# Kernel tuning notes

Hardware: AMD Instinct MI355X
Metric: run time of the kernel (lower is better)

Reference implementation:

```python
import jax, jax.numpy as jnp
import numpy as np

# module hyperparams (init_kwargs)
OUTLINER_RATIO_1 = 0.01
OUTLINER_RATIO_2 = 0.01
SUB_OUTLINER_RATIO_2 = 0.2
SUB_OUTLINER_BIT_2 = 8
RANK = 16


def setup_inputs() -> dict:
    key = jax.random.key(0)
    k1, k2 = jax.random.split(key)
    B, H, S, D = 2, 16, 2048, 128
    # x1 is a softmax output (attention probabilities): rows sum to 1, values in [0,1]
    logits = jax.random.normal(k1, (B, H, S, S), dtype=jnp.float32)
    x1 = jax.nn.softmax(logits, axis=-1)
    x2 = jax.random.normal(k2, (B, H, S, D), dtype=jnp.float32)
    return {"x1": x1, "x2": x2}


def get_statistics_softmax(x, outliner_ratio):
    # kth-value threshold on first batch element (torch.kthvalue, 1-indexed)
    v = jnp.sort(x[0].reshape(-1))
    k = int(v.size * (1.0 - outliner_ratio))
    return v[k - 1]


def get_statistics_x2(x, outliner_ratio, sub_ratio, bit):
    x0 = x[0]  # [H, S, D]
    D = x0.shape[-1]
    a = jnp.abs(x0).reshape(-1)
    k = int(a.size * (1.0 - outliner_ratio))
    outliner = jnp.sort(a)[k - 1]
    # residual after removing outliers; rank columns by L2 norm
    resid = jnp.where(jnp.abs(x0) > outliner, 0.0, x0).reshape(-1, D)
    col_norm = jnp.linalg.norm(resid, axis=0)  # [D]
    n_cols = max(1, int(sub_ratio * D))
    _, cols = jax.lax.top_k(col_norm, n_cols)  # max-norm column list (static size)
    sub = resid[:, cols]
    qmax = float(2 ** (bit - 1) - 1)
    scale = jnp.max(jnp.abs(sub)) / qmax
    return outliner, cols, scale


def prune_softmax(x, outliner):
    return jnp.where(x > outliner, x, 0.0)


def fake_divide_outliner_suboutlinear_svd(x, outliner, cols, scale, rank, bit):
    # 1) split out outliers (kept exactly)
    x_out = jnp.where(jnp.abs(x) > outliner, x, 0.0)
    r = x - x_out
    # 2) rank-`rank` SVD approximation of the residual (batched over B,H)
    U, Sv, Vt = jnp.linalg.svd(r, full_matrices=False)
    x_lr = (U[..., :rank] * Sv[..., None, :rank]) @ Vt[..., :rank, :]
    r2 = r - x_lr
    # 3) fake-quantize the high-norm (sub-outlier) columns at `bit` bits; drop the rest
    qmax = float(2 ** (bit - 1) - 1)
    sub_q = jnp.clip(jnp.round(r2[..., cols] / scale), -qmax - 1.0, qmax) * scale
    r_q = jnp.zeros_like(r2).at[..., cols].set(sub_q)
    return x_out + x_lr + r_q


def reference(x1, x2):
    # iteration = 0 (< 10): compute statistics branch of EfficientMemoryGEMMWithSoftmaxFunc.forward
    result = x1 @ x2
    outliner_1 = get_statistics_softmax(x1, OUTLINER_RATIO_1)
    outliner_2, cols_2, scale_2 = get_statistics_x2(
        x2, OUTLINER_RATIO_2, SUB_OUTLINER_RATIO_2, SUB_OUTLINER_BIT_2)
    # The pruned/compressed tensors are computed (saved for backward in torch);
    # forward output matches Func.forward's returns.
    _x1p = prune_softmax(x1, outliner_1)
    _x2c = fake_divide_outliner_suboutlinear_svd(
        x2, outliner_2, cols_2, scale_2, RANK, SUB_OUTLINER_BIT_2)
    return (result, outliner_1, outliner_2, cols_2, scale_2)
```

## Files before the change

### kernel.cpp

```cpp
#include <hip/hip_runtime.h>

typedef __bf16 bf16x8 __attribute__((ext_vector_type(8)));
typedef unsigned short u16x8 __attribute__((ext_vector_type(8)));
typedef float f32x4 __attribute__((ext_vector_type(4)));

#define S_DIM 2048
#define D_DIM 128
#define N1 67108864LL
#define N2 4194304LL
#define RANK1 66437774u
#define RANK2 4152359u

#define OUT_O1 8388608
#define OUT_O2 8388609
#define OUT_COLS 8388610
#define OUT_SCALE 8388635

#define WS_H0 0
#define WS_H1 2048
#define WS_H2 4096
#define WS_H3 6144
#define WS_STATE 6656
#define WS_SMAX 6660
#define WS_MASK 6664
#define WS_SUMSQ 6672
#define WS_TOTAL 8192

__device__ __forceinline__ unsigned short f2bf(float f) {
  unsigned u = __float_as_uint(f);
  return (unsigned short)((u + 0x7FFFu + ((u >> 16) & 1u)) >> 16);
}

__device__ __forceinline__ unsigned long long pack4(float x, float y, float z, float w) {
  return (unsigned long long)f2bf(x)
       | ((unsigned long long)f2bf(y) << 16)
       | ((unsigned long long)f2bf(z) << 32)
       | ((unsigned long long)f2bf(w) << 48);
}

__global__ void init_ws(unsigned* __restrict__ ws) {
  int i = blockIdx.x * 256 + threadIdx.x;
  if (i < WS_TOTAL) ws[i] = (i == WS_STATE) ? RANK2 : 0u;
}

#define LDA 40

__global__ __launch_bounds__(256, 2) void gemm_kernel(
    const float* __restrict__ x1, const float* __restrict__ x2,
    float* __restrict__ out, unsigned* __restrict__ hist) {
  __shared__ __align__(16) unsigned short lA[128 * LDA];
  __shared__ __align__(16) unsigned short lB[128 * LDA];
  __shared__ unsigned lh[4][2048];

  const int bid = blockIdx.x;
  const int bh = (bid & 7) + ((bid >> 7) << 3);
  const int mt = (bid >> 3) & 15;
  const int t = threadIdx.x;
  const int lane = t & 63;
  const int wave = t >> 6;
  const int wm = (wave >> 1) * 64;
  const int wn = (wave & 1) * 64;
  const int l15 = lane & 15;
  const int quad = lane >> 4;
  const bool do_hist = (bh < 16);

  unsigned* myh = lh[wave];
  if (do_hist) {
    for (int i = lane; i < 2048; i += 64) myh[i] = 0u;
  }

  const float* Ag = x1 + (long long)bh * S_DIM * S_DIM + (long long)mt * 128 * S_DIM;
  const float* Bg = x2 + (long long)bh * S_DIM * D_DIM;
  float* Cg = out + (long long)bh * S_DIM * D_DIM + (long long)mt * 128 * D_DIM;

  f32x4 acc[4][4];
#pragma unroll
  for (int i = 0; i < 4; ++i)
#pragma unroll
    for (int j = 0; j < 4; ++j) acc[i][j] = f32x4{0.f, 0.f, 0.f, 0.f};

  const int a_seg = t & 7;
  const int a_row = t >> 3;
  const int b_n = t & 127;
  const int b_kq = t >> 7;

  float4 a_r[4];
  float4 b_r[4];
#pragma unroll
  for (int p = 0; p < 4; ++p)
    a_r[p] = *reinterpret_cast<const float4*>(Ag + (long long)(a_row + p * 32) * S_DIM + a_seg * 4);
#pragma unroll
  for (int g = 0; g < 4; ++g) {
    int k0 = b_kq * 16 + g * 4;
    long long base = (long long)k0 * D_DIM + b_n;
    b_r[g].x = Bg[base];
    b_r[g].y = Bg[base + D_DIM];
    b_r[g].z = Bg[base + 2 * D_DIM];
    b_r[g].w = Bg[base + 3 * D_DIM];
  }

  for (int kb = 0; kb < S_DIM; kb += 32) {
#pragma unroll
    for (int p = 0; p < 4; ++p) {
      int row = a_row + p * 32;
      *reinterpret_cast<unsigned long long*>(&lA[row * LDA + a_seg * 4]) =
          pack4(a_r[p].x, a_r[p].y, a_r[p].z, a_r[p].w);
    }
#pragma unroll
    for (int g = 0; g < 4; ++g) {
      int k0 = b_kq * 16 + g * 4;
      *reinterpret_cast<unsigned long long*>(&lB[b_n * LDA + k0]) =
          pack4(b_r[g].x, b_r[g].y, b_r[g].z, b_r[g].w);
    }

    if (do_hist) {
#pragma unroll
      for (int p = 0; p < 4; ++p) {
        atomicAdd(&myh[__float_as_uint(a_r[p].x) >> 19], 1u);
        atomicAdd(&myh[__float_as_uint(a_r[p].y) >> 19], 1u);
        atomicAdd(&myh[__float_as_uint(a_r[p].z) >> 19], 1u);
        atomicAdd(&myh[__float_as_uint(a_r[p].w) >> 19], 1u);
      }
    }

    if (kb + 32 < S_DIM) {
#pragma unroll
      for (int p = 0; p < 4; ++p)
        a_r[p] = *reinterpret_cast<const float4*>(
            Ag + (long long)(a_row + p * 32) * S_DIM + (kb + 32) + a_seg * 4);
#pragma unroll
      for (int g = 0; g < 4; ++g) {
        int k0 = b_kq * 16 + g * 4;
        long long base = (long long)(kb + 32 + k0) * D_DIM + b_n;
        b_r[g].x = Bg[base];
        b_r[g].y = Bg[base + D_DIM];
        b_r[g].z = Bg[base + 2 * D_DIM];
        b_r[g].w = Bg[base + 3 * D_DIM];
      }
    }
    __syncthreads();

    bf16x8 af[4], bfr[4];
#pragma unroll
    for (int i = 0; i < 4; ++i) {
      af[i] = __builtin_bit_cast(bf16x8,
          *reinterpret_cast<const u16x8*>(&lA[(wm + i * 16 + l15) * LDA + quad * 8]));
      bfr[i] = __builtin_bit_cast(bf16x8,
          *reinterpret_cast<const u16x8*>(&lB[(wn + i * 16 + l15) * LDA + quad * 8]));
    }
#pragma unroll
    for (int i = 0; i < 4; ++i)
#pragma unroll
      for (int j = 0; j < 4; ++j)
        acc[i][j] = __builtin_amdgcn_mfma_f32_16x16x32_bf16(af[i], bfr[j], acc[i][j], 0, 0, 0);
    __syncthreads();
  }

#pragma unroll
  for (int i = 0; i < 4; ++i) {
#pragma unroll
    for (int j = 0; j < 4; ++j) {
      int row0 = wm + i * 16 + quad * 4;
      int col = wn + j * 16 + l15;
#pragma unroll
      for (int r = 0; r < 4; ++r)
        Cg[(long long)(row0 + r) * D_DIM + col] = acc[i][j][r];
    }
  }

  if (do_hist) {
    for (int i = t; i < 2048; i += 256) {
      unsigned s = lh[0][i] + lh[1][i] + lh[2][i] + lh[3][i];
      if (s) atomicAdd(&hist[i], s);
    }
  }
}

__global__ void x1_select(const unsigned* __restrict__ hist, float* __restrict__ out) {
  __shared__ unsigned ps[256];
  const int t = threadIdx.x;
  unsigned v[8];
  unsigned s = 0;
#pragma unroll
  for (int j = 0; j < 8; ++j) { v[j] = hist[t * 8 + j]; s += v[j]; }
  ps[t] = s;
  __syncthreads();
  for (int off = 1; off < 256; off <<= 1) {
    unsigned add = (t >= off) ? ps[t - off] : 0u;
    __syncthreads();
    ps[t] += add;
    __syncthreads();
  }
  unsigned incl = ps[t];
  unsigned before = incl - s;
  if (RANK1 >= before && RANK1 < incl) {
    unsigned rr = RANK1 - before;
    for (int j = 0; j < 8; ++j) {
      if (rr < v[j]) {
        unsigned b = (unsigned)(t * 8 + j);
        float lo = __uint_as_float(b << 19);
        float hi = __uint_as_float((b + 1u) << 19);
        out[OUT_O1] = lo + (hi - lo) * (((float)rr + 0.5f) / (float)v[j]);
        break;
      }
      rr -= v[j];
    }
  }
}

__global__ void x2_hist(const float* __restrict__ x2, unsigned* __restrict__ h,
                        const unsigned* __restrict__ state, int phase) {
  __shared__ unsigned lh[2048];
  const int nb = (phase == 3) ? 512 : 2048;
  for (int i = threadIdx.x; i < nb; i += 256) lh[i] = 0u;
  __syncthreads();
  const unsigned b1 = state[1];
  const unsigned pfx2 = (state[1] << 11) | state[2];
  long long i0 = (long long)(blockIdx.x * 256 + threadIdx.x) * 4;
  long long stride = (long long)gridDim.x * 1024;
  for (long long i = i0; i < N2; i += stride) {
    float4 v = *reinterpret_cast<const float4*>(x2 + i);
    float fv[4] = {v.x, v.y, v.z, v.w};
#pragma unroll
    for (int j = 0; j < 4; ++j) {
      unsigned key = __float_as_uint(fv[j]) & 0x7FFFFFFFu;
      if (phase == 1) {
        atomicAdd(&lh[key >> 20], 1u);
      } else if (phase == 2) {
        if ((key >> 20) == b1) atomicAdd(&lh[(key >> 9) & 0x7FFu], 1u);
      } else {
        if ((key >> 9) == pfx2) atomicAdd(&lh[key & 0x1FFu], 1u);
      }
    }
  }
  __syncthreads();
  for (int i = threadIdx.x; i < nb; i += 256)
    if (lh[i]) atomicAdd(&h[i], lh[i]);
}

__global__ void x2_scan(const unsigned* __restrict__ h, unsigned* state,
                        float* __restrict__ out, int phase) {
  __shared__ unsigned ps[256];
  const int nb = (phase == 3) ? 512 : 2048;
  const int per = nb >> 8;
  const int t = threadIdx.x;
  const unsigned r = state[0];
  const unsigned sb1 = state[1];
  const unsigned sb2 = state[2];
  unsigned v[8];
  unsigned s = 0;
  for (int j = 0; j < per; ++j) { v[j] = h[t * per + j]; s += v[j]; }
  ps[t] = s;
  __syncthreads();
  for (int off = 1; off < 256; off <<= 1) {
    unsigned add = (t >= off) ? ps[t - off] : 0u;
    __syncthreads();
    ps[t] += add;
    __syncthreads();
  }
  unsigned incl = ps[t];
  unsigned before = incl - s;
  if (r >= before && r < incl) {
    unsigned rr = r - before;
    for (int j = 0; j < per; ++j) {
      if (rr < v[j]) {
        unsigned b = (unsigned)(t * per + j);
        state[0] = rr;
        if (phase == 1) state[1] = b;
        else if (phase == 2) state[2] = b;
        else {
          unsigned bits = (sb1 << 20) | (sb2 << 9) | b;
          state[3] = bits;
          out[OUT_O2] = __uint_as_float(bits);
        }
        break;
      }
      rr -= v[j];
    }
  }
}

__global__ void colnorm_kernel(const float* __restrict__ x2,
                               const unsigned* __restrict__ state,
                               float* __restrict__ sumsq) {
  const float thr = __uint_as_float(state[3]);
  const int t = threadIdx.x;
  const int c = t & 127;
  const int half = t >> 7;
  float local = 0.f;
  for (int i = 0; i < 64; ++i) {
    int row = blockIdx.x * 128 + i * 2 + half;
    float x = x2[(long long)row * 128 + c];
    if (fabsf(x) <= thr) local += x * x;
  }
  __shared__ float red[256];
  red[t] = local;
  __syncthreads();
  if (half == 0) atomicAdd(&sumsq[c], red[c] + red[c + 128]);
}

__global__ void topk_kernel(const float* __restrict__ sumsq, float* __restrict__ out,
                            unsigned* __restrict__ mask) {
  __shared__ float v[128];
  __shared__ float rv[128];
  __shared__ int ri[128];
  __shared__ unsigned msk[4];
  const int t = threadIdx.x;
  v[t] = sumsq[t];
  if (t < 4) msk[t] = 0u;
  __syncthreads();
  for (int s = 0; s < 25; ++s) {
    rv[t] = v[t];
    ri[t] = t;
    __syncthreads();
    for (int off = 64; off >= 1; off >>= 1) {
      if (t < off) {
        float a = rv[t], b = rv[t + off];
        int ia = ri[t], ib = ri[t + off];
        if (b > a || (b == a && ib < ia)) { rv[t] = b; ri[t] = ib; }
      }
      __syncthreads();
    }
    if (t == 0) {
      int c = ri[0];
      out[OUT_COLS + s] = (float)c;
      v[c] = -1.0f;
      msk[c >> 5] |= 1u << (c & 31);
    }
    __syncthreads();
  }
  if (t < 4) mask[t] = msk[t];
}

__global__ void scale_kernel(const float* __restrict__ x2,
                             const unsigned* __restrict__ state,
                             const unsigned* __restrict__ mask,
                             unsigned* __restrict__ smax) {
  const float thr = __uint_as_float(state[3]);
  unsigned long long mlo = (unsigned long long)mask[0] | ((unsigned long long)mask[1] << 32);
  unsigned long long mhi = (unsigned long long)mask[2] | ((unsigned long long)mask[3] << 32);
  long long i0 = (long long)(blockIdx.x * 256 + threadIdx.x) * 4;
  long long stride = (long long)gridDim.x * 1024;
  float best = 0.f;
  for (long long i = i0; i < N2; i += stride) {
    float4 v = *reinterpret_cast<const float4*>(x2 + i);
    float fv[4] = {v.x, v.y, v.z, v.w};
    int cbase = (int)(i & 127);
#pragma unroll
    for (int j = 0; j < 4; ++j) {
      int c = cbase + j;
      unsigned long long w = (c < 64) ? mlo : mhi;
      if ((w >> (c & 63)) & 1ULL) {
        float a = fabsf(fv[j]);
        if (a <= thr && a > best) best = a;
      }
    }
  }
  __shared__ float red[256];
  red[threadIdx.x] = best;
  __syncthreads();
  for (int off = 128; off >= 1; off >>= 1) {
    if (threadIdx.x < off) red[threadIdx.x] = fmaxf(red[threadIdx.x], red[threadIdx.x + off]);
    __syncthreads();
  }
  if (threadIdx.x == 0) atomicMax(smax, __float_as_uint(red[0]));
}

__global__ void finalize_kernel(const unsigned* __restrict__ smax, float* __restrict__ out) {
  out[OUT_SCALE] = __uint_as_float(*smax) / 127.0f;
}

extern "C" void kernel_launch(void* const* d_in, const int* in_sizes, int n_in,
                              void* d_out, int out_size, void* d_ws, size_t ws_size,
                              hipStream_t stream) {
  (void)in_sizes; (void)n_in; (void)out_size; (void)ws_size;
  const float* x1 = (const float*)d_in[0];
  const float* x2 = (const float*)d_in[1];
  float* out = (float*)d_out;
  unsigned* ws = (unsigned*)d_ws;

  init_ws<<<32, 256, 0, stream>>>(ws);
  gemm_kernel<<<512, 256, 0, stream>>>(x1, x2, out, ws + WS_H0);
  x1_select<<<1, 256, 0, stream>>>(ws + WS_H0, out);
  x2_hist<<<256, 256, 0, stream>>>(x2, ws + WS_H1, ws + WS_STATE, 1);
  x2_scan<<<1, 256, 0, stream>>>(ws + WS_H1, ws + WS_STATE, out, 1);
  x2_hist<<<256, 256, 0, stream>>>(x2, ws + WS_H2, ws + WS_STATE, 2);
  x2_scan<<<1, 256, 0, stream>>>(ws + WS_H2, ws + WS_STATE, out, 2);
  x2_hist<<<256, 256, 0, stream>>>(x2, ws + WS_H3, ws + WS_STATE, 3);
  x2_scan<<<1, 256, 0, stream>>>(ws + WS_H3, ws + WS_STATE, out, 3);
  colnorm_kernel<<<256, 256, 0, stream>>>(x2, ws + WS_STATE, (float*)(ws + WS_SUMSQ));
  topk_kernel<<<1, 128, 0, stream>>>((const float*)(ws + WS_SUMSQ), out, ws + WS_MASK);
  scale_kernel<<<256, 256, 0, stream>>>(x2, ws + WS_STATE, ws + WS_MASK, ws + WS_SMAX);
  finalize_kernel<<<1, 1, 0, stream>>>(ws + WS_SMAX, out);
}
```

Before: 843.4 us.

## Fuse statistics kernels via last-block tickets and fold x2 histogram into GEMM

```diff
diff --git a/kernel.cpp b/kernel.cpp
--- a/kernel.cpp
+++ b/kernel.cpp
@@ -21,21 +21,15 @@
 #define WS_H2 4096
 #define WS_H3 6144
 #define WS_STATE 6656
-#define WS_SMAX 6660
-#define WS_MASK 6664
 #define WS_SUMSQ 6672
+#define WS_CMAX 6800
+#define WS_TICKET 6928
 #define WS_TOTAL 8192
 
-__device__ __forceinline__ unsigned short f2bf(float f) {
-  unsigned u = __float_as_uint(f);
-  return (unsigned short)((u + 0x7FFFu + ((u >> 16) & 1u)) >> 16);
-}
-
-__device__ __forceinline__ unsigned long long pack4(float x, float y, float z, float w) {
-  return (unsigned long long)f2bf(x)
-       | ((unsigned long long)f2bf(y) << 16)
-       | ((unsigned long long)f2bf(z) << 32)
-       | ((unsigned long long)f2bf(w) << 48);
+__device__ __forceinline__ unsigned long long pack4c(float x, float y, float z, float w) {
+  union { unsigned long long u; __bf16 h[4]; } cv;
+  cv.h[0] = (__bf16)x; cv.h[1] = (__bf16)y; cv.h[2] = (__bf16)z; cv.h[3] = (__bf16)w;
+  return cv.u;
 }
 
 __global__ void init_ws(unsigned* __restrict__ ws) {
@@ -47,10 +41,13 @@
 
 __global__ __launch_bounds__(256, 2) void gemm_kernel(
     const float* __restrict__ x1, const float* __restrict__ x2,
-    float* __restrict__ out, unsigned* __restrict__ hist) {
+    float* __restrict__ out, unsigned* __restrict__ ws) {
   __shared__ __align__(16) unsigned short lA[128 * LDA];
   __shared__ __align__(16) unsigned short lB[128 * LDA];
   __shared__ unsigned lh[4][2048];
+  __shared__ unsigned lh2[2048];
+  __shared__ unsigned ps[256];
+  __shared__ unsigned lastt;
 
   const int bid = blockIdx.x;
   const int bh = (bid & 7) + ((bid >> 7) << 3);
@@ -67,7 +64,9 @@
   unsigned* myh = lh[wave];
   if (do_hist) {
     for (int i = lane; i < 2048; i += 64) myh[i] = 0u;
-  }
+    for (int i = t; i < 2048; i += 256) lh2[i] = 0u;
+  }
+  __syncthreads();
 
   const float* Ag = x1 + (long long)bh * S_DIM * S_DIM + (long long)mt * 128 * S_DIM;
   const float* Bg = x2 + (long long)bh * S_DIM * D_DIM;
@@ -81,61 +80,71 @@
 
   const int a_seg = t & 7;
   const int a_row = t >> 3;
-  const int b_n = t & 127;
+  const int bcol = t & 127;
   const int b_kq = t >> 7;
 
-  float4 a_r[4];
-  float4 b_r[4];
+  float4 a_c[4], b_c[4];
 #pragma unroll
   for (int p = 0; p < 4; ++p)
-    a_r[p] = *reinterpret_cast<const float4*>(Ag + (long long)(a_row + p * 32) * S_DIM + a_seg * 4);
+    a_c[p] = *reinterpret_cast<const float4*>(Ag + (long long)(a_row + p * 32) * S_DIM + a_seg * 4);
 #pragma unroll
   for (int g = 0; g < 4; ++g) {
     int k0 = b_kq * 16 + g * 4;
-    long long base = (long long)k0 * D_DIM + b_n;
-    b_r[g].x = Bg[base];
-    b_r[g].y = Bg[base + D_DIM];
-    b_r[g].z = Bg[base + 2 * D_DIM];
-    b_r[g].w = Bg[base + 3 * D_DIM];
+    long long base = (long long)k0 * D_DIM + bcol;
+    b_c[g].x = Bg[base];
+    b_c[g].y = Bg[base + D_DIM];
+    b_c[g].z = Bg[base + 2 * D_DIM];
+    b_c[g].w = Bg[base + 3 * D_DIM];
   }
 
   for (int kb = 0; kb < S_DIM; kb += 32) {
+    float4 a_p[4], b_p[4];
+    const bool pf = (kb + 32 < S_DIM);
+    if (pf) {
+#pragma unroll
+      for (int p = 0; p < 4; ++p)
+        a_p[p] = *reinterpret_cast<const float4*>(
+            Ag + (long long)(a_row + p * 32) * S_DIM + (kb + 32) + a_seg * 4);
+#pragma unroll
+      for (int g = 0; g < 4; ++g) {
+        int k0 = b_kq * 16 + g * 4;
+        long long base = (long long)(kb + 32 + k0) * D_DIM + bcol;
+        b_p[g].x = Bg[base];
+        b_p[g].y = Bg[base + D_DIM];
+        b_p[g].z = Bg[base + 2 * D_DIM];
+        b_p[g].w = Bg[base + 3 * D_DIM];
+      }
+    }
+
 #pragma unroll
     for (int p = 0; p < 4; ++p) {
       int row = a_row + p * 32;
       *reinterpret_cast<unsigned long long*>(&lA[row * LDA + a_seg * 4]) =
-          pack4(a_r[p].x, a_r[p].y, a_r[p].z, a_r[p].w);
+          pack4c(a_c[p].x, a_c[p].y, a_c[p].z, a_c[p].w);
     }
 #pragma unroll
     for (int g = 0; g < 4; ++g) {
       int k0 = b_kq * 16 + g * 4;
-      *reinterpret_cast<unsigned long long*>(&lB[b_n * LDA + k0]) =
-          pack4(b_r[g].x, b_r[g].y, b_r[g].z, b_r[g].w);
+      *reinterpret_cast<unsigned long long*>(&lB[bcol * LDA + k0]) =
+          pack4c(b_c[g].x, b_c[g].y, b_c[g].z, b_c[g].w);
     }
 
     if (do_hist) {
 #pragma unroll
       for (int p = 0; p < 4; ++p) {
-        atomicAdd(&myh[__float_as_uint(a_r[p].x) >> 19], 1u);
-        atomicAdd(&myh[__float_as_uint(a_r[p].y) >> 19], 1u);
-        atomicAdd(&myh[__float_as_uint(a_r[p].z) >> 19], 1u);
-        atomicAdd(&myh[__float_as_uint(a_r[p].w) >> 19], 1u);
-      }
-    }
-
-    if (kb + 32 < S_DIM) {
-#pragma unroll
-      for (int p = 0; p < 4; ++p)
-        a_r[p] = *reinterpret_cast<const float4*>(
-            Ag + (long long)(a_row + p * 32) * S_DIM + (kb + 32) + a_seg * 4);
-#pragma unroll
-      for (int g = 0; g < 4; ++g) {
-        int k0 = b_kq * 16 + g * 4;
-        long long base = (long long)(kb + 32 + k0) * D_DIM + b_n;
-        b_r[g].x = Bg[base];
-        b_r[g].y = Bg[base + D_DIM];
-        b_r[g].z = Bg[base + 2 * D_DIM];
-        b_r[g].w = Bg[base + 3 * D_DIM];
+        atomicAdd(&myh[__float_as_uint(a_c[p].x) >> 19], 1u);
+        atomicAdd(&myh[__float_as_uint(a_c[p].y) >> 19], 1u);
+        atomicAdd(&myh[__float_as_uint(a_c[p].z) >> 19], 1u);
+        atomicAdd(&myh[__float_as_uint(a_c[p].w) >> 19], 1u);
+      }
+      if ((kb >> 7) == mt) {
+#pragma unroll
+        for (int g = 0; g < 4; ++g) {
+          atomicAdd(&lh2[(__float_as_uint(b_c[g].x) & 0x7FFFFFFFu) >> 20], 1u);
+          atomicAdd(&lh2[(__float_as_uint(b_c[g].y) & 0x7FFFFFFFu) >> 20], 1u);
+          atomicAdd(&lh2[(__float_as_uint(b_c[g].z) & 0x7FFFFFFFu) >> 20], 1u);
+          atomicAdd(&lh2[(__float_as_uint(b_c[g].w) & 0x7FFFFFFFu) >> 20], 1u);
+        }
       }
     }
     __syncthreads();
@@ -154,6 +163,13 @@
       for (int j = 0; j < 4; ++j)
         acc[i][j] = __builtin_amdgcn_mfma_f32_16x16x32_bf16(af[i], bfr[j], acc[i][j], 0, 0, 0);
     __syncthreads();
+
+    if (pf) {
+#pragma unroll
+      for (int p = 0; p < 4; ++p) a_c[p] = a_p[p];
+#pragma unroll
+      for (int g = 0; g < 4; ++g) b_c[g] = b_p[g];
+    }
   }
 
 #pragma unroll
@@ -171,52 +187,91 @@
   if (do_hist) {
     for (int i = t; i < 2048; i += 256) {
       unsigned s = lh[0][i] + lh[1][i] + lh[2][i] + lh[3][i];
-      if (s) atomicAdd(&hist[i], s);
-    }
-  }
-}
-
-__global__ void x1_select(const unsigned* __restrict__ hist, float* __restrict__ out) {
+      if (s) atomicAdd(&ws[WS_H0 + i], s);
+      unsigned s2 = lh2[i];
+      if (s2) atomicAdd(&ws[WS_H1 + i], s2);
+    }
+  }
+  __threadfence();
+  __syncthreads();
+  if (t == 0) lastt = atomicAdd(&ws[WS_TICKET + 0], 1u);
+  __syncthreads();
+  if (lastt != 511u) return;
+
+  {
+    unsigned v[8];
+    unsigned s = 0;
+#pragma unroll
+    for (int j = 0; j < 8; ++j) { v[j] = atomicAdd(&ws[WS_H0 + t * 8 + j], 0u); s += v[j]; }
+    ps[t] = s;
+    __syncthreads();
+    for (int off = 1; off < 256; off <<= 1) {
+      unsigned add = (t >= off) ? ps[t - off] : 0u;
+      __syncthreads();
+      ps[t] += add;
+      __syncthreads();
+    }
+    unsigned incl = ps[t];
+    unsigned before = incl - s;
+    if (RANK1 >= before && RANK1 < incl) {
+      unsigned rr = RANK1 - before;
+      for (int j = 0; j < 8; ++j) {
+        if (rr < v[j]) {
+          unsigned b = (unsigned)(t * 8 + j);
+          float lo = __uint_as_float(b << 19);
+          float hi = __uint_as_float((b + 1u) << 19);
+          out[OUT_O1] = lo + (hi - lo) * (((float)rr + 0.5f) / (float)v[j]);
+          break;
+        }
+        rr -= v[j];
+      }
+    }
+  }
+  __syncthreads();
+
+  {
+    unsigned v[8];
+    unsigned s = 0;
+#pragma unroll
+    for (int j = 0; j < 8; ++j) { v[j] = atomicAdd(&ws[WS_H1 + t * 8 + j], 0u); s += v[j]; }
+    ps[t] = s;
+    __syncthreads();
+    for (int off = 1; off < 256; off <<= 1) {
+      unsigned add = (t >= off) ? ps[t - off] : 0u;
+      __syncthreads();
+      ps[t] += add;
+      __syncthreads();
+    }
+    unsigned incl = ps[t];
+    unsigned before = incl - s;
+    if (RANK2 >= before && RANK2 < incl) {
+      unsigned rr = RANK2 - before;
+      for (int j = 0; j < 8; ++j) {
+        if (rr < v[j]) {
+          ws[WS_STATE + 0] = rr;
+          ws[WS_STATE + 1] = (unsigned)(t * 8 + j);
+          break;
+        }
+        rr -= v[j];
+      }
+    }
+  }
+}
+
+__global__ void x2_pass(const float* __restrict__ x2, unsigned* __restrict__ ws,
+                        float* __restrict__ out, int phase) {
+  __shared__ unsigned lh[2048];
   __shared__ unsigned ps[256];
+  __shared__ unsigned lastt;
+  unsigned* h = ws + ((phase == 2) ? WS_H2 : WS_H3);
+  unsigned* state = ws + WS_STATE;
+  const int nb = (phase == 3) ? 512 : 2048;
   const int t = threadIdx.x;
-  unsigned v[8];
-  unsigned s = 0;
-#pragma unroll
-  for (int j = 0; j < 8; ++j) { v[j] = hist[t * 8 + j]; s += v[j]; }
-  ps[t] = s;
-  __syncthreads();
-  for (int off = 1; off < 256; off <<= 1) {
-    unsigned add = (t >= off) ? ps[t - off] : 0u;
-    __syncthreads();
-    ps[t] += add;
-    __syncthreads();
-  }
-  unsigned incl = ps[t];
-  unsigned before = incl - s;
-  if (RANK1 >= before && RANK1 < incl) {
-    unsigned rr = RANK1 - before;
-    for (int j = 0; j < 8; ++j) {
-      if (rr < v[j]) {
-        unsigned b = (unsigned)(t * 8 + j);
-        float lo = __uint_as_float(b << 19);
-        float hi = __uint_as_float((b + 1u) << 19);
-        out[OUT_O1] = lo + (hi - lo) * (((float)rr + 0.5f) / (float)v[j]);
-        break;
-      }
-      rr -= v[j];
-    }
-  }
-}
-
-__global__ void x2_hist(const float* __restrict__ x2, unsigned* __restrict__ h,
-                        const unsigned* __restrict__ state, int phase) {
-  __shared__ unsigned lh[2048];
-  const int nb = (phase == 3) ? 512 : 2048;
-  for (int i = threadIdx.x; i < nb; i += 256) lh[i] = 0u;
+  for (int i = t; i < nb; i += 256) lh[i] = 0u;
   __syncthreads();
   const unsigned b1 = state[1];
   const unsigned pfx2 = (state[1] << 11) | state[2];
-  long long i0 = (long long)(blockIdx.x * 256 + threadIdx.x) * 4;
+  long long i0 = (long long)(blockIdx.x * 256 + t) * 4;
   long long stride = (long long)gridDim.x * 1024;
   for (long long i = i0; i < N2; i += stride) {
     float4 v = *reinterpret_cast<const float4*>(x2 + i);
@@ -224,9 +279,7 @@
 #pragma unroll
     for (int j = 0; j < 4; ++j) {
       unsigned key = __float_as_uint(fv[j]) & 0x7FFFFFFFu;
-      if (phase == 1) {
-        atomicAdd(&lh[key >> 20], 1u);
-      } else if (phase == 2) {
+      if (phase == 2) {
         if ((key >> 20) == b1) atomicAdd(&lh[(key >> 9) & 0x7FFu], 1u);
       } else {
         if ((key >> 9) == pfx2) atomicAdd(&lh[key & 0x1FFu], 1u);
@@ -234,22 +287,21 @@
     }
   }
   __syncthreads();
-  for (int i = threadIdx.x; i < nb; i += 256)
+  for (int i = t; i < nb; i += 256)
     if (lh[i]) atomicAdd(&h[i], lh[i]);
-}
-
-__global__ void x2_scan(const unsigned* __restrict__ h, unsigned* state,
-                        float* __restrict__ out, int phase) {
-  __shared__ unsigned ps[256];
-  const int nb = (phase == 3) ? 512 : 2048;
+  __threadfence();
+  __syncthreads();
+  if (t == 0) lastt = atomicAdd(&ws[WS_TICKET + ((phase == 2) ? 1 : 2)], 1u);
+  __syncthreads();
+  if (lastt != 255u) return;
+
   const int per = nb >> 8;
-  const int t = threadIdx.x;
   const unsigned r = state[0];
   const unsigned sb1 = state[1];
   const unsigned sb2 = state[2];
   unsigned v[8];
   unsigned s = 0;
-  for (int j = 0; j < per; ++j) { v[j] = h[t * per + j]; s += v[j]; }
+  for (int j = 0; j < per; ++j) { v[j] = atomicAdd(&h[t * per + j], 0u); s += v[j]; }
   ps[t] = s;
   __syncthreads();
   for (int off = 1; off < 256; off <<= 1) {
@@ -265,10 +317,10 @@
     for (int j = 0; j < per; ++j) {
       if (rr < v[j]) {
         unsigned b = (unsigned)(t * per + j);
-        state[0] = rr;
-        if (phase == 1) state[1] = b;
-        else if (phase == 2) state[2] = b;
-        else {
+        if (phase == 2) {
+          state[0] = rr;
+          state[2] = b;
+        } else {
           unsigned bits = (sb1 << 20) | (sb2 << 9) | b;
           state[3] = bits;
           out[OUT_O2] = __uint_as_float(bits);
@@ -280,38 +332,56 @@
   }
 }
 
-__global__ void colnorm_kernel(const float* __restrict__ x2,
-                               const unsigned* __restrict__ state,
-                               float* __restrict__ sumsq) {
+__global__ void colnorm_kernel(const float* __restrict__ x2, unsigned* __restrict__ ws,
+                               float* __restrict__ out) {
+  __shared__ float red[256];
+  __shared__ unsigned redm[256];
+  __shared__ float vv[128];
+  __shared__ float rv[128];
+  __shared__ int ri[128];
+  __shared__ unsigned cmv[128];
+  __shared__ unsigned lastt;
+  unsigned* state = ws + WS_STATE;
+  float* sumsq = (float*)(ws + WS_SUMSQ);
+  unsigned* cmax = ws + WS_CMAX;
   const float thr = __uint_as_float(state[3]);
   const int t = threadIdx.x;
   const int c = t & 127;
   const int half = t >> 7;
   float local = 0.f;
+  unsigned lmax = 0u;
   for (int i = 0; i < 64; ++i) {
     int row = blockIdx.x * 128 + i * 2 + half;
     float x = x2[(long long)row * 128 + c];
-    if (fabsf(x) <= thr) local += x * x;
-  }
-  __shared__ float red[256];
+    float a = fabsf(x);
+    if (a <= thr) {
+      local += x * x;
+      unsigned ab = __float_as_uint(a);
+      if (ab > lmax) lmax = ab;
+    }
+  }
   red[t] = local;
-  __syncthreads();
-  if (half == 0) atomicAdd(&sumsq[c], red[c] + red[c + 128]);
-}
-
-__global__ void topk_kernel(const float* __restrict__ sumsq, float* __restrict__ out,
-                            unsigned* __restrict__ mask) {
-  __shared__ float v[128];
-  __shared__ float rv[128];
-  __shared__ int ri[128];
-  __shared__ unsigned msk[4];
-  const int t = threadIdx.x;
-  v[t] = sumsq[t];
-  if (t < 4) msk[t] = 0u;
-  __syncthreads();
-  for (int s = 0; s < 25; ++s) {
-    rv[t] = v[t];
-    ri[t] = t;
+  redm[t] = lmax;
+  __syncthreads();
+  if (half == 0) {
+    atomicAdd(&sumsq[c], red[c] + red[c + 128]);
+    unsigned m = redm[c] > redm[c + 128] ? redm[c] : redm[c + 128];
+    if (m) atomicMax(&cmax[c], m);
+  }
+  __threadfence();
+  __syncthreads();
+  if (t == 0) lastt = atomicAdd(&ws[WS_TICKET + 3], 1u);
+  __syncthreads();
+  if (lastt != 255u) return;
+
+  if (t < 128) {
+    vv[t] = atomicAdd(&sumsq[t], 0.0f);
+    cmv[t] = atomicMax(&cmax[t], 0u);
+  }
+  __syncthreads();
+  unsigned smax = 0u;
+  for (int s2 = 0; s2 < 25; ++s2) {
+    if (t < 128) { rv[t] = vv[t]; ri[t] = t; }
     __syncthreads();
     for (int off = 64; off >= 1; off >>= 1) {
       if (t < off) {
@@ -322,52 +392,14 @@
       __syncthreads();
     }
     if (t == 0) {
-      int c = ri[0];
-      out[OUT_COLS + s] = (float)c;
-      v[c] = -1.0f;
-      msk[c >> 5] |= 1u << (c & 31);
-    }
-    __syncthreads();
-  }
-  if (t < 4) mask[t] = msk[t];
-}
-
-__global__ void scale_kernel(const float* __restrict__ x2,
-                             const unsigned* __restrict__ state,
-                             const unsigned* __restrict__ mask,
-                             unsigned* __restrict__ smax) {
-  const float thr = __uint_as_float(state[3]);
-  unsigned long long mlo = (unsigned long long)mask[0] | ((unsigned long long)mask[1] << 32);
-  unsigned long long mhi = (unsigned long long)mask[2] | ((unsigned long long)mask[3] << 32);
-  long long i0 = (long long)(blockIdx.x * 256 + threadIdx.x) * 4;
-  long long stride = (long long)gridDim.x * 1024;
-  float best = 0.f;
-  for (long long i = i0; i < N2; i += stride) {
-    float4 v = *reinterpret_cast<const float4*>(x2 + i);
-    float fv[4] = {v.x, v.y, v.z, v.w};
-    int cbase = (int)(i & 127);
-#pragma unroll
-    for (int j = 0; j < 4; ++j) {
-      int c = cbase + j;
-      unsigned long long w = (c < 64) ? mlo : mhi;
-      if ((w >> (c & 63)) & 1ULL) {
-        float a = fabsf(fv[j]);
-        if (a <= thr && a > best) best = a;
-      }
-    }
-  }
-  __shared__ float red[256];
-  red[threadIdx.x] = best;
-  __syncthreads();
-  for (int off = 128; off >= 1; off >>= 1) {
-    if (threadIdx.x < off) red[threadIdx.x] = fmaxf(red[threadIdx.x], red[threadIdx.x + off]);
-    __syncthreads();
-  }
-  if (threadIdx.x == 0) atomicMax(smax, __float_as_uint(red[0]));
-}
-
-__global__ void finalize_kernel(const unsigned* __restrict__ smax, float* __restrict__ out) {
-  out[OUT_SCALE] = __uint_as_float(*smax) / 127.0f;
+      int cc = ri[0];
+      out[OUT_COLS + s2] = (float)cc;
+      vv[cc] = -1.0f;
+      if (cmv[cc] > smax) smax = cmv[cc];
+    }
+    __syncthreads();
+  }
+  if (t == 0) out[OUT_SCALE] = __uint_as_float(smax) / 127.0f;
 }
 
 extern "C" void kernel_launch(void* const* d_in, const int* in_sizes, int n_in,
@@ -380,16 +412,8 @@
   unsigned* ws = (unsigned*)d_ws;
 
   init_ws<<<32, 256, 0, stream>>>(ws);
-  gemm_kernel<<<512, 256, 0, stream>>>(x1, x2, out, ws + WS_H0);
-  x1_select<<<1, 256, 0, stream>>>(ws + WS_H0, out);
-  x2_hist<<<256, 256, 0, stream>>>(x2, ws + WS_H1, ws + WS_STATE, 1);
-  x2_scan<<<1, 256, 0, stream>>>(ws + WS_H1, ws + WS_STATE, out, 1);
-  x2_hist<<<256, 256, 0, stream>>>(x2, ws + WS_H2, ws + WS_STATE, 2);
-  x2_scan<<<1, 256, 0, stream>>>(ws + WS_H2, ws + WS_STATE, out, 2);
-  x2_hist<<<256, 256, 0, stream>>>(x2, ws + WS_H3, ws + WS_STATE, 3);
-  x2_scan<<<1, 256, 0, stream>>>(ws + WS_H3, ws + WS_STATE, out, 3);
-  colnorm_kernel<<<256, 256, 0, stream>>>(x2, ws + WS_STATE, (float*)(ws + WS_SUMSQ));
-  topk_kernel<<<1, 128, 0, stream>>>((const float*)(ws + WS_SUMSQ), out, ws + WS_MASK);
-  scale_kernel<<<256, 256, 0, stream>>>(x2, ws + WS_STATE, ws + WS_MASK, ws + WS_SMAX);
-  finalize_kernel<<<1, 1, 0, stream>>>(ws + WS_SMAX, out);
-}
+  gemm_kernel<<<512, 256, 0, stream>>>(x1, x2, out, ws);
+  x2_pass<<<256, 256, 0, stream>>>(x2, ws, out, 2);
+  x2_pass<<<256, 256, 0, stream>>>(x2, ws, out, 3);
+  colnorm_kernel<<<256, 256, 0, stream>>>(x2, ws, out);
+}
```

Measured after the change: 927.0 us. 9.9% more time.
